# Optimization experiments

Measured on AMD Instinct MI355X. Metric: run time of the kernel, lower is better.

Reference implementation:

```python
import jax, jax.numpy as jnp
import numpy as np

B, N, D_IN, D_OUT, R = 8, 1024, 256, 256, 4


def setup_inputs() -> dict:
    key = jax.random.key(0)
    ks = jax.random.split(key, 8)
    scale_in = 1.0 / np.sqrt(D_IN)
    scale_out = 1.0 / np.sqrt(2 * D_OUT)
    scale_g = 1.0 / np.sqrt(D_OUT)
    return {
        "node_features": jax.random.normal(ks[0], (B, N, D_IN), dtype=jnp.float32),
        "adj_matrix": jax.random.randint(ks[1], (B, R, N, N), 0, 2, dtype=jnp.int32),
        "rel_w": jax.random.uniform(ks[2], (R, D_OUT, D_IN), jnp.float32, -scale_in, scale_in),
        "rel_b": jax.random.uniform(ks[3], (R, D_OUT), jnp.float32, -scale_in, scale_in),
        "attn_w": jax.random.uniform(ks[4], (2 * D_OUT,), jnp.float32, -scale_out, scale_out),
        "attn_b": jax.random.uniform(ks[5], (), jnp.float32, -scale_out, scale_out),
        "gate_w": jax.random.uniform(ks[6], (D_OUT,), jnp.float32, -scale_g, scale_g),
        "gate_b": jax.random.uniform(ks[7], (), jnp.float32, -scale_g, scale_g),
    }


def reference(node_features, adj_matrix, rel_w, rel_b, attn_w, attn_b, gate_w, gate_b):
    # Per-relation projections: [B, R, N, D]
    feats = jnp.einsum('bni,rdi->brnd', node_features, rel_w) + rel_b[None, :, None, :]
    # attn_proj(cat([h_i, h_j])) == h_i @ w_i + h_j @ w_j + b  (linear over concat)
    d = feats.shape[-1]
    si = jnp.einsum('brnd,d->brn', feats, attn_w[:d])   # contribution of row node i
    sj = jnp.einsum('brnd,d->brn', feats, attn_w[d:])   # contribution of col node j
    score = si[:, :, :, None] + sj[:, :, None, :] + attn_b  # [B, R, N, N]
    score = jnp.where(adj_matrix == 0, jnp.float32(-1e9), score)
    attn = jax.nn.softmax(score, axis=-1)
    # Aggregate over relations: sum_r attn_r @ feats_r -> [B, N, D]
    agg = jnp.einsum('brnm,brmd->bnd', attn, feats)
    gate = jax.nn.sigmoid(jnp.einsum('bnd,d->bn', agg, gate_w) + gate_b)
    return gate[:, :, None] * agg
```

## Files before the change

### kernel.cpp

```cpp
#include <hip/hip_runtime.h>
#include <hip/hip_bf16.h>

#define B_ 8
#define N_ 1024
#define DIN 256
#define DOUT 256
#define R_ 4

typedef __attribute__((ext_vector_type(8))) short bf16x8;
typedef __attribute__((ext_vector_type(4))) float f32x4;
typedef __attribute__((ext_vector_type(4))) int i32x4;

__device__ __forceinline__ unsigned short f2bf(float f) {
    union { float f; unsigned int u; } v; v.f = f;
    unsigned int u = v.u;
    u += 0x7fffu + ((u >> 16) & 1u);
    return (unsigned short)(u >> 16);
}
__device__ __forceinline__ float bf2f(unsigned short h) {
    union { float f; unsigned int u; } v; v.u = ((unsigned int)h) << 16;
    return v.f;
}

__device__ __forceinline__ void gl_lds16(const void* g, void* l) {
    __builtin_amdgcn_global_load_lds(
        (const __attribute__((address_space(1))) unsigned int*)g,
        (__attribute__((address_space(3))) unsigned int*)l, 16, 0, 0);
}

__global__ __launch_bounds__(256) void k0_swz(const float* __restrict__ rw,
                                              unsigned short* __restrict__ swzW) {
    int t = blockIdx.x * 256 + threadIdx.x;
    int lane = t & 63, nb = (t >> 6) & 15, ks = (t >> 10) & 7, r = t >> 13;
    int m = lane & 15, q = lane >> 4;
    const float* src = rw + ((r * DOUT + nb * 16 + m) * DIN) + ks * 32 + q * 8;
    float4 v0 = *(const float4*)src;
    float4 v1 = *(const float4*)(src + 4);
    bf16x8 o;
    o[0] = (short)f2bf(v0.x); o[1] = (short)f2bf(v0.y);
    o[2] = (short)f2bf(v0.z); o[3] = (short)f2bf(v0.w);
    o[4] = (short)f2bf(v1.x); o[5] = (short)f2bf(v1.y);
    o[6] = (short)f2bf(v1.z); o[7] = (short)f2bf(v1.w);
    *(bf16x8*)(swzW + (long)t * 8) = o;
}

__global__ __launch_bounds__(256) void k1_proj(const float* __restrict__ node,
        const unsigned short* __restrict__ swzW, const float* __restrict__ rel_b,
        const float* __restrict__ attn_w,
        unsigned short* __restrict__ fswz, unsigned short* __restrict__ ebf) {
    __shared__ unsigned short Wbuf[2][8192];
    int bid = blockIdx.x;
    int nt = bid & 15, r = (bid >> 4) & 3, b = bid >> 6;
    int w = threadIdx.x >> 6, lane = threadIdx.x & 63;
    int m = lane & 15, q = lane >> 4;
    int n0 = nt * 64 + w * 16;

    const float* Abase = node + ((b * N_ + n0 + m) * DIN) + q * 8;
    const unsigned short* Wsrc = swzW + r * 65536;

#pragma unroll
    for (int i = 0; i < 4; i++)
        gl_lds16(Wsrc + (w * 4 + i) * 512 + lane * 8, &Wbuf[0][(w * 4 + i) * 512]);

    f32x4 acc[16];
#pragma unroll
    for (int i = 0; i < 16; i++) acc[i] = (f32x4)0.0f;

    float4 a0 = *(const float4*)(Abase);
    float4 a1 = *(const float4*)(Abase + 4);

    for (int ks = 0; ks < 8; ks++) {
        int cur = ks & 1;
        __syncthreads();
        if (ks < 7) {
#pragma unroll
            for (int i = 0; i < 4; i++)
                gl_lds16(Wsrc + ((ks + 1) * 16 + w * 4 + i) * 512 + lane * 8,
                         &Wbuf[cur ^ 1][(w * 4 + i) * 512]);
        }
        bf16x8 af;
        af[0] = (short)f2bf(a0.x); af[1] = (short)f2bf(a0.y);
        af[2] = (short)f2bf(a0.z); af[3] = (short)f2bf(a0.w);
        af[4] = (short)f2bf(a1.x); af[5] = (short)f2bf(a1.y);
        af[6] = (short)f2bf(a1.z); af[7] = (short)f2bf(a1.w);
        if (ks < 7) {
            a0 = *(const float4*)(Abase + (ks + 1) * 32);
            a1 = *(const float4*)(Abase + (ks + 1) * 32 + 4);
        }
#pragma unroll
        for (int nb = 0; nb < 16; nb++) {
            bf16x8 wf = *(const bf16x8*)(&Wbuf[cur][nb * 512 + lane * 8]);
            acc[nb] = __builtin_amdgcn_mfma_f32_16x16x32_bf16(af, wf, acc[nb], 0, 0, 0);
        }
    }

    float sj0 = 0.f, sj1 = 0.f, sj2 = 0.f, sj3 = 0.f;
    float bias[16], aw[16];
#pragma unroll
    for (int nb = 0; nb < 16; nb++) {
        int d = nb * 16 + m;
        bias[nb] = rel_b[r * DOUT + d];
        aw[nb] = attn_w[DOUT + d];
        sj0 += (acc[nb][0] + bias[nb]) * aw[nb];
        sj1 += (acc[nb][1] + bias[nb]) * aw[nb];
        sj2 += (acc[nb][2] + bias[nb]) * aw[nb];
        sj3 += (acc[nb][3] + bias[nb]) * aw[nb];
    }
#pragma unroll
    for (int mk = 1; mk <= 8; mk <<= 1) {
        sj0 += __shfl_xor(sj0, mk, 64);
        sj1 += __shfl_xor(sj1, mk, 64);
        sj2 += __shfl_xor(sj2, mk, 64);
        sj3 += __shfl_xor(sj3, mk, 64);
    }
    float e0 = __expf(sj0), e1 = __expf(sj1), e2 = __expf(sj2), e3 = __expf(sj3);

    int slice = b * R_ + r;
    int js = n0 >> 5;
    int jhi = (n0 >> 4) & 1;
    int qp = jhi * 2 + (q >> 1);
    int jj0 = (q & 1) * 4;
    unsigned short* fb = fswz + ((long)(slice * 32 + js) * 16) * 512
                       + qp * 128 + m * 8 + jj0;
#pragma unroll
    for (int nb = 0; nb < 16; nb++) {
        ushort4 o;
        o.x = f2bf((acc[nb][0] + bias[nb]) * e0);
        o.y = f2bf((acc[nb][1] + bias[nb]) * e1);
        o.z = f2bf((acc[nb][2] + bias[nb]) * e2);
        o.w = f2bf((acc[nb][3] + bias[nb]) * e3);
        *(ushort4*)(fb + nb * 512) = o;
    }
    if (m == 0) {
        ushort4 o;
        o.x = f2bf(e0); o.y = f2bf(e1); o.z = f2bf(e2); o.w = f2bf(e3);
        *(ushort4*)(ebf + slice * N_ + n0 + q * 4) = o;
    }
}

__global__ __launch_bounds__(256, 4) void k3_attn(const int* __restrict__ adj,
        const unsigned short* __restrict__ fswz, const unsigned short* __restrict__ ebf,
        unsigned short* __restrict__ aggN) {
    __shared__ unsigned short Gbuf[2][8192];
    __shared__ unsigned short Ebuf[1024];
    __shared__ float Lx[2][64];

    int bid = blockIdx.x;
    int slice = (bid & 7) * 4 + ((bid >> 3) & 3);
    int it = bid >> 5;
    int t = threadIdx.x, lane = t & 63, w = t >> 6;
    int m = lane & 15, q = lane >> 4;
    int g = w & 1;
    int ph = w >> 1;
    int i0 = it * 32 + g * 16;

    const unsigned short* fsl = fswz + (size_t)slice * (32 * 8192);
    const int* adjbase = adj + (size_t)slice * (N_ * N_)
                       + (size_t)(i0 + m) * N_ + q * 8;
    const unsigned short* esl = ebf + slice * N_;

#pragma unroll
    for (int i = 0; i < 4; i++)
        gl_lds16(fsl + (w * 4 + i) * 512 + lane * 8, &Gbuf[0][(w * 4 + i) * 512]);
    if (w < 2)
        gl_lds16(esl + w * 512 + lane * 8, &Ebuf[w * 512]);

    i32x4 A0c = *(const i32x4*)(adjbase + ph * 32);
    i32x4 A1c = *(const i32x4*)(adjbase + ph * 32 + 4);

    f32x4 acc[16];
#pragma unroll
    for (int i = 0; i < 16; i++) acc[i] = (f32x4)0.0f;
    float l = 0.f;

    for (int s = 0; s < 32; s++) {
        int cur = s & 1;
        __syncthreads();
        if (s < 31) {
#pragma unroll
            for (int i = 0; i < 4; i++)
                gl_lds16(fsl + (size_t)(s + 1) * 8192 + (w * 4 + i) * 512 + lane * 8,
                         &Gbuf[cur ^ 1][(w * 4 + i) * 512]);
        }
        if ((s & 1) == ph) {
            i32x4 A0n, A1n;
            if (s < 30) {
                A0n = *(const i32x4*)(adjbase + (s + 2) * 32);
                A1n = *(const i32x4*)(adjbase + (s + 2) * 32 + 4);
            }
            bf16x8 ev = *(const bf16x8*)(&Ebuf[s * 32 + q * 8]);
            int av[8] = {A0c.x, A0c.y, A0c.z, A0c.w, A1c.x, A1c.y, A1c.z, A1c.w};
            const int* ei = (const int*)&ev;
            bf16x8 af;
            int* afi = (int*)&af;
#pragma unroll
            for (int p = 0; p < 4; p++) {
                unsigned int msk = (av[2 * p] ? 0xffffu : 0u)
                                 | (av[2 * p + 1] ? 0xffff0000u : 0u);
                afi[p] = (int)(msk & 0x3F803F80u);
                int me = ei[p] & (int)msk;
                union { int i; float f; } lo, hi;
                lo.i = me << 16;
                hi.i = me & (int)0xffff0000u;
                l += lo.f + hi.f;
            }
            const unsigned short* Gb = &Gbuf[cur][lane * 8];
#pragma unroll
            for (int nb = 0; nb < 16; nb++) {
                bf16x8 bfq = *(const bf16x8*)(Gb + nb * 512);
                acc[nb] = __builtin_amdgcn_mfma_f32_16x16x32_bf16(af, bfq, acc[nb], 0, 0, 0);
            }
            if (s < 30) { A0c = A0n; A1c = A1n; }
        }
    }

    __syncthreads();
    if (w >= 2) {
        float* GF = (float*)&Gbuf[0][0];
#pragma unroll
        for (int nb = 0; nb < 16; nb++)
            *(f32x4*)(&GF[g * 4096 + nb * 256 + lane * 4]) = acc[nb];
        Lx[g][lane] = l;
    }
    __syncthreads();
    if (w < 2) {
        const float* GF = (const float*)&Gbuf[0][0];
#pragma unroll
        for (int nb = 0; nb < 16; nb++)
            acc[nb] += *(const f32x4*)(&GF[g * 4096 + nb * 256 + lane * 4]);
        l += Lx[g][lane];
        l += __shfl_xor(l, 16, 64);
        l += __shfl_xor(l, 32, 64);
        float linv[4];
#pragma unroll
        for (int reg = 0; reg < 4; reg++) {
            float lr = __shfl(l, q * 4 + reg, 64);
            linv[reg] = (lr > 0.f) ? 1.0f / lr : 0.f;
        }
        unsigned short* ob = aggN + ((size_t)(slice * N_ + i0 + q * 4)) * DOUT + m;
#pragma unroll
        for (int nb = 0; nb < 16; nb++) {
#pragma unroll
            for (int reg = 0; reg < 4; reg++)
                ob[(size_t)reg * DOUT + nb * 16] = f2bf(acc[nb][reg] * linv[reg]);
        }
    }
}

__global__ __launch_bounds__(256) void k4_out(const unsigned short* __restrict__ aggN,
        const float* __restrict__ gate_w, const float* __restrict__ gate_b,
        float* __restrict__ out) {
    __shared__ float red[4];
    int bid = blockIdx.x;
    int n = bid & 1023, b = bid >> 10;
    int d = threadIdx.x;
    float s = 0.f;
#pragma unroll
    for (int r = 0; r < R_; r++)
        s += bf2f(aggN[((size_t)((b * R_ + r) * N_ + n)) * DOUT + d]);
    float v = s * gate_w[d];
#pragma unroll
    for (int off = 32; off; off >>= 1) v += __shfl_down(v, off, 64);
    int lane = d & 63, wave = d >> 6;
    if (lane == 0) red[wave] = v;
    __syncthreads();
    float tot = red[0] + red[1] + red[2] + red[3];
    float g = 1.f / (1.f + __expf(-(tot + gate_b[0])));
    out[((size_t)(b * N_ + n)) * DOUT + d] = g * s;
}

extern "C" void kernel_launch(void* const* d_in, const int* in_sizes, int n_in,
                              void* d_out, int out_size, void* d_ws, size_t ws_size,
                              hipStream_t stream) {
    const float* node   = (const float*)d_in[0];
    const int*   adj    = (const int*)d_in[1];
    const float* rel_w  = (const float*)d_in[2];
    const float* rel_b  = (const float*)d_in[3];
    const float* attn_w = (const float*)d_in[4];
    const float* gate_w = (const float*)d_in[6];
    const float* gate_b = (const float*)d_in[7];
    float* out = (float*)d_out;

    char* ws = (char*)d_ws;
    unsigned short* swzW = (unsigned short*)ws;
    unsigned short* fswz = (unsigned short*)(ws + 524288);
    unsigned short* ebf  = (unsigned short*)(ws + 17301504);
    unsigned short* aggN = (unsigned short*)(ws + 17367040);

    k0_swz<<<128, 256, 0, stream>>>(rel_w, swzW);
    k1_proj<<<512, 256, 0, stream>>>(node, swzW, rel_b, attn_w, fswz, ebf);
    k3_attn<<<1024, 256, 0, stream>>>(adj, fswz, ebf, aggN);
    k4_out<<<8192, 256, 0, stream>>>(aggN, gate_w, gate_b, out);
}
```

Baseline: 257.1 us.

## Restructure attention kernel: 64 rows per block, 4-slot pipeline with vmcnt waits

The attention kernel now gives each of its four waves a distinct 16-row tile, so a block covers 64 rows and the grid is halved. This replaces the old scheme where pairs of waves split the column steps and then merged partial sums through shared memory. Feature tiles and adjacency loads move into a 4-slot LDS/register ring, prefetched two steps ahead. Manual s_waitcnt vmcnt plus raw barriers replace __syncthreads so loads in flight can stay pending. Each fswz tile is now reused across more rows, at the cost of more LDS per block (occupancy bound lowered to 2) and fragile hand-counted waitcnt logic.

```diff
diff --git a/kernel.cpp b/kernel.cpp
--- a/kernel.cpp
+++ b/kernel.cpp
@@ -26,6 +26,12 @@
     __builtin_amdgcn_global_load_lds(
         (const __attribute__((address_space(1))) unsigned int*)g,
         (__attribute__((address_space(3))) unsigned int*)l, 16, 0, 0);
+}
+
+__device__ __forceinline__ i32x4 gload4(const void* p) {
+    i32x4 r;
+    asm volatile("global_load_dwordx4 %0, %1, off" : "=v"(r) : "v"(p) : "memory");
+    return r;
 }
 
 __global__ __launch_bounds__(256) void k0_swz(const float* __restrict__ rw,
@@ -138,112 +144,105 @@
     }
 }
 
-__global__ __launch_bounds__(256, 4) void k3_attn(const int* __restrict__ adj,
+#define K3_STEP(T_, SLOT_, PFSLOT_, DO_PF_, WAITN_)                            \
+  {                                                                            \
+    asm volatile("s_waitcnt vmcnt(" #WAITN_ ")" ::: "memory");                 \
+    __builtin_amdgcn_s_barrier();                                              \
+    __builtin_amdgcn_sched_barrier(0);                                         \
+    if (DO_PF_) {                                                              \
+      _Pragma("unroll")                                                        \
+      for (int i = 0; i < 4; i++)                                              \
+        gl_lds16(fsl + (size_t)((T_) + 2) * 8192 + (w * 4 + i) * 512 + lane * 8, \
+                 &Gbuf[PFSLOT_][(w * 4 + i) * 512]);                           \
+      adjA[PFSLOT_] = gload4(adjbase + ((T_) + 2) * 32);                       \
+      adjB[PFSLOT_] = gload4(adjbase + ((T_) + 2) * 32 + 4);                   \
+    }                                                                          \
+    bf16x8 ev = *(const bf16x8*)(&Ebuf[(T_) * 32 + q * 8]);                    \
+    i32x4 A0c = adjA[SLOT_], A1c = adjB[SLOT_];                                \
+    int av[8] = {A0c.x, A0c.y, A0c.z, A0c.w, A1c.x, A1c.y, A1c.z, A1c.w};      \
+    const int* ei = (const int*)&ev;                                           \
+    bf16x8 af; int* afi = (int*)&af;                                           \
+    _Pragma("unroll")                                                          \
+    for (int p = 0; p < 4; p++) {                                              \
+      unsigned int msk = (av[2 * p] ? 0xffffu : 0u)                            \
+                       | (av[2 * p + 1] ? 0xffff0000u : 0u);                   \
+      afi[p] = (int)(msk & 0x3F803F80u);                                       \
+      int me = ei[p] & (int)msk;                                               \
+      union { int i; float f; } lo, hi;                                        \
+      lo.i = me << 16; hi.i = me & (int)0xffff0000u;                           \
+      l += lo.f + hi.f;                                                        \
+    }                                                                          \
+    const unsigned short* Gb = &Gbuf[SLOT_][lane * 8];                         \
+    _Pragma("unroll")                                                          \
+    for (int nb = 0; nb < 16; nb++) {                                          \
+      bf16x8 bfq = *(const bf16x8*)(Gb + nb * 512);                            \
+      acc[nb] = __builtin_amdgcn_mfma_f32_16x16x32_bf16(af, bfq, acc[nb], 0, 0, 0); \
+    }                                                                          \
+  }
+
+__global__ __launch_bounds__(256, 2) void k3_attn(const int* __restrict__ adj,
         const unsigned short* __restrict__ fswz, const unsigned short* __restrict__ ebf,
         unsigned short* __restrict__ aggN) {
-    __shared__ unsigned short Gbuf[2][8192];
+    __shared__ unsigned short Gbuf[4][8192];
     __shared__ unsigned short Ebuf[1024];
-    __shared__ float Lx[2][64];
 
     int bid = blockIdx.x;
     int slice = (bid & 7) * 4 + ((bid >> 3) & 3);
     int it = bid >> 5;
     int t = threadIdx.x, lane = t & 63, w = t >> 6;
     int m = lane & 15, q = lane >> 4;
-    int g = w & 1;
-    int ph = w >> 1;
-    int i0 = it * 32 + g * 16;
+    int i0 = it * 64 + w * 16;
 
     const unsigned short* fsl = fswz + (size_t)slice * (32 * 8192);
     const int* adjbase = adj + (size_t)slice * (N_ * N_)
                        + (size_t)(i0 + m) * N_ + q * 8;
     const unsigned short* esl = ebf + slice * N_;
 
+    i32x4 adjA[4], adjB[4];
+
 #pragma unroll
     for (int i = 0; i < 4; i++)
         gl_lds16(fsl + (w * 4 + i) * 512 + lane * 8, &Gbuf[0][(w * 4 + i) * 512]);
     if (w < 2)
         gl_lds16(esl + w * 512 + lane * 8, &Ebuf[w * 512]);
-
-    i32x4 A0c = *(const i32x4*)(adjbase + ph * 32);
-    i32x4 A1c = *(const i32x4*)(adjbase + ph * 32 + 4);
+    adjA[0] = gload4(adjbase);
+    adjB[0] = gload4(adjbase + 4);
+#pragma unroll
+    for (int i = 0; i < 4; i++)
+        gl_lds16(fsl + 8192 + (w * 4 + i) * 512 + lane * 8, &Gbuf[1][(w * 4 + i) * 512]);
+    adjA[1] = gload4(adjbase + 32);
+    adjB[1] = gload4(adjbase + 36);
 
     f32x4 acc[16];
 #pragma unroll
     for (int i = 0; i < 16; i++) acc[i] = (f32x4)0.0f;
     float l = 0.f;
 
-    for (int s = 0; s < 32; s++) {
-        int cur = s & 1;
-        __syncthreads();
-        if (s < 31) {
-#pragma unroll
-            for (int i = 0; i < 4; i++)
-                gl_lds16(fsl + (size_t)(s + 1) * 8192 + (w * 4 + i) * 512 + lane * 8,
-                         &Gbuf[cur ^ 1][(w * 4 + i) * 512]);
-        }
-        if ((s & 1) == ph) {
-            i32x4 A0n, A1n;
-            if (s < 30) {
-                A0n = *(const i32x4*)(adjbase + (s + 2) * 32);
-                A1n = *(const i32x4*)(adjbase + (s + 2) * 32 + 4);
-            }
-            bf16x8 ev = *(const bf16x8*)(&Ebuf[s * 32 + q * 8]);
-            int av[8] = {A0c.x, A0c.y, A0c.z, A0c.w, A1c.x, A1c.y, A1c.z, A1c.w};
-            const int* ei = (const int*)&ev;
-            bf16x8 af;
-            int* afi = (int*)&af;
-#pragma unroll
-            for (int p = 0; p < 4; p++) {
-                unsigned int msk = (av[2 * p] ? 0xffffu : 0u)
-                                 | (av[2 * p + 1] ? 0xffff0000u : 0u);
-                afi[p] = (int)(msk & 0x3F803F80u);
-                int me = ei[p] & (int)msk;
-                union { int i; float f; } lo, hi;
-                lo.i = me << 16;
-                hi.i = me & (int)0xffff0000u;
-                l += lo.f + hi.f;
-            }
-            const unsigned short* Gb = &Gbuf[cur][lane * 8];
-#pragma unroll
-            for (int nb = 0; nb < 16; nb++) {
-                bf16x8 bfq = *(const bf16x8*)(Gb + nb * 512);
-                acc[nb] = __builtin_amdgcn_mfma_f32_16x16x32_bf16(af, bfq, acc[nb], 0, 0, 0);
-            }
-            if (s < 30) { A0c = A0n; A1c = A1n; }
-        }
-    }
-
-    __syncthreads();
-    if (w >= 2) {
-        float* GF = (float*)&Gbuf[0][0];
-#pragma unroll
-        for (int nb = 0; nb < 16; nb++)
-            *(f32x4*)(&GF[g * 4096 + nb * 256 + lane * 4]) = acc[nb];
-        Lx[g][lane] = l;
-    }
-    __syncthreads();
-    if (w < 2) {
-        const float* GF = (const float*)&Gbuf[0][0];
-#pragma unroll
-        for (int nb = 0; nb < 16; nb++)
-            acc[nb] += *(const f32x4*)(&GF[g * 4096 + nb * 256 + lane * 4]);
-        l += Lx[g][lane];
-        l += __shfl_xor(l, 16, 64);
-        l += __shfl_xor(l, 32, 64);
-        float linv[4];
-#pragma unroll
-        for (int reg = 0; reg < 4; reg++) {
-            float lr = __shfl(l, q * 4 + reg, 64);
-            linv[reg] = (lr > 0.f) ? 1.0f / lr : 0.f;
-        }
-        unsigned short* ob = aggN + ((size_t)(slice * N_ + i0 + q * 4)) * DOUT + m;
-#pragma unroll
-        for (int nb = 0; nb < 16; nb++) {
-#pragma unroll
-            for (int reg = 0; reg < 4; reg++)
-                ob[(size_t)reg * DOUT + nb * 16] = f2bf(acc[nb][reg] * linv[reg]);
-        }
+    for (int tt = 0; tt < 28; tt += 4) {
+        K3_STEP(tt + 0, 0, 2, 1, 6)
+        K3_STEP(tt + 1, 1, 3, 1, 6)
+        K3_STEP(tt + 2, 2, 0, 1, 6)
+        K3_STEP(tt + 3, 3, 1, 1, 6)
+    }
+    K3_STEP(28, 0, 2, 1, 6)
+    K3_STEP(29, 1, 3, 1, 6)
+    K3_STEP(30, 2, 0, 0, 6)
+    K3_STEP(31, 3, 1, 0, 0)
+
+    l += __shfl_xor(l, 16, 64);
+    l += __shfl_xor(l, 32, 64);
+    float linv[4];
+#pragma unroll
+    for (int reg = 0; reg < 4; reg++) {
+        float lr = __shfl(l, q * 4 + reg, 64);
+        linv[reg] = (lr > 0.f) ? 1.0f / lr : 0.f;
+    }
+    unsigned short* ob = aggN + ((size_t)(slice * N_ + i0 + q * 4)) * DOUT + m;
+#pragma unroll
+    for (int nb = 0; nb < 16; nb++) {
+#pragma unroll
+        for (int reg = 0; reg < 4; reg++)
+            ob[(size_t)reg * DOUT + nb * 16] = f2bf(acc[nb][reg] * linv[reg]);
     }
 }
 
@@ -289,6 +288,6 @@
 
     k0_swz<<<128, 256, 0, stream>>>(rel_w, swzW);
     k1_proj<<<512, 256, 0, stream>>>(node, swzW, rel_b, attn_w, fswz, ebf);
-    k3_attn<<<1024, 256, 0, stream>>>(adj, fswz, ebf, aggN);
+    k3_attn<<<512, 256, 0, stream>>>(adj, fswz, ebf, aggN);
     k4_out<<<8192, 256, 0, stream>>>(aggN, gate_w, gate_b, out);
 }
```

New measurement: 251.6 us. -2.2%, faster.

## Restructure attention kernel: each wave owns 16 rows, read features directly from global

Applied to the files above, without the earlier changes.

The attention aggregation kernel is reorganised so that each of the four waves handles its own 16 query rows across all 32 key tiles. This removes the split-K phase scheme, the cross-wave LDS reduction and the per-step barriers. Feature tiles are now read straight from global memory (relying on L2/cache) instead of being double-buffered through LDS. The grid is halved to 512 blocks and the occupancy hint drops to 2. This trades LDS traffic and synchronisation for more redundant global/L2 reads of the features per block and less latency hiding.

```diff
diff --git a/kernel.cpp b/kernel.cpp
--- a/kernel.cpp
+++ b/kernel.cpp
@@ -138,112 +138,78 @@
     }
 }
 
-__global__ __launch_bounds__(256, 4) void k3_attn(const int* __restrict__ adj,
+__global__ __launch_bounds__(256, 2) void k3_attn(const int* __restrict__ adj,
         const unsigned short* __restrict__ fswz, const unsigned short* __restrict__ ebf,
         unsigned short* __restrict__ aggN) {
-    __shared__ unsigned short Gbuf[2][8192];
     __shared__ unsigned short Ebuf[1024];
-    __shared__ float Lx[2][64];
 
     int bid = blockIdx.x;
     int slice = (bid & 7) * 4 + ((bid >> 3) & 3);
     int it = bid >> 5;
     int t = threadIdx.x, lane = t & 63, w = t >> 6;
     int m = lane & 15, q = lane >> 4;
-    int g = w & 1;
-    int ph = w >> 1;
-    int i0 = it * 32 + g * 16;
+    int i0 = it * 64 + w * 16;
 
     const unsigned short* fsl = fswz + (size_t)slice * (32 * 8192);
     const int* adjbase = adj + (size_t)slice * (N_ * N_)
                        + (size_t)(i0 + m) * N_ + q * 8;
-    const unsigned short* esl = ebf + slice * N_;
-
-#pragma unroll
-    for (int i = 0; i < 4; i++)
-        gl_lds16(fsl + (w * 4 + i) * 512 + lane * 8, &Gbuf[0][(w * 4 + i) * 512]);
-    if (w < 2)
-        gl_lds16(esl + w * 512 + lane * 8, &Ebuf[w * 512]);
-
-    i32x4 A0c = *(const i32x4*)(adjbase + ph * 32);
-    i32x4 A1c = *(const i32x4*)(adjbase + ph * 32 + 4);
+
+    ((ushort4*)Ebuf)[t] = ((const ushort4*)(ebf + slice * N_))[t];
+    __syncthreads();
 
     f32x4 acc[16];
 #pragma unroll
     for (int i = 0; i < 16; i++) acc[i] = (f32x4)0.0f;
     float l = 0.f;
 
+    i32x4 A0c = *(const i32x4*)(adjbase);
+    i32x4 A1c = *(const i32x4*)(adjbase + 4);
+
     for (int s = 0; s < 32; s++) {
-        int cur = s & 1;
-        __syncthreads();
+        i32x4 A0n, A1n;
         if (s < 31) {
-#pragma unroll
-            for (int i = 0; i < 4; i++)
-                gl_lds16(fsl + (size_t)(s + 1) * 8192 + (w * 4 + i) * 512 + lane * 8,
-                         &Gbuf[cur ^ 1][(w * 4 + i) * 512]);
-        }
-        if ((s & 1) == ph) {
-            i32x4 A0n, A1n;
-            if (s < 30) {
-                A0n = *(const i32x4*)(adjbase + (s + 2) * 32);
-                A1n = *(const i32x4*)(adjbase + (s + 2) * 32 + 4);
-            }
-            bf16x8 ev = *(const bf16x8*)(&Ebuf[s * 32 + q * 8]);
-            int av[8] = {A0c.x, A0c.y, A0c.z, A0c.w, A1c.x, A1c.y, A1c.z, A1c.w};
-            const int* ei = (const int*)&ev;
-            bf16x8 af;
-            int* afi = (int*)&af;
-#pragma unroll
-            for (int p = 0; p < 4; p++) {
-                unsigned int msk = (av[2 * p] ? 0xffffu : 0u)
-                                 | (av[2 * p + 1] ? 0xffff0000u : 0u);
-                afi[p] = (int)(msk & 0x3F803F80u);
-                int me = ei[p] & (int)msk;
-                union { int i; float f; } lo, hi;
-                lo.i = me << 16;
-                hi.i = me & (int)0xffff0000u;
-                l += lo.f + hi.f;
-            }
-            const unsigned short* Gb = &Gbuf[cur][lane * 8];
-#pragma unroll
-            for (int nb = 0; nb < 16; nb++) {
-                bf16x8 bfq = *(const bf16x8*)(Gb + nb * 512);
-                acc[nb] = __builtin_amdgcn_mfma_f32_16x16x32_bf16(af, bfq, acc[nb], 0, 0, 0);
-            }
-            if (s < 30) { A0c = A0n; A1c = A1n; }
-        }
-    }
-
-    __syncthreads();
-    if (w >= 2) {
-        float* GF = (float*)&Gbuf[0][0];
-#pragma unroll
-        for (int nb = 0; nb < 16; nb++)
-            *(f32x4*)(&GF[g * 4096 + nb * 256 + lane * 4]) = acc[nb];
-        Lx[g][lane] = l;
-    }
-    __syncthreads();
-    if (w < 2) {
-        const float* GF = (const float*)&Gbuf[0][0];
-#pragma unroll
-        for (int nb = 0; nb < 16; nb++)
-            acc[nb] += *(const f32x4*)(&GF[g * 4096 + nb * 256 + lane * 4]);
-        l += Lx[g][lane];
-        l += __shfl_xor(l, 16, 64);
-        l += __shfl_xor(l, 32, 64);
-        float linv[4];
-#pragma unroll
-        for (int reg = 0; reg < 4; reg++) {
-            float lr = __shfl(l, q * 4 + reg, 64);
-            linv[reg] = (lr > 0.f) ? 1.0f / lr : 0.f;
-        }
-        unsigned short* ob = aggN + ((size_t)(slice * N_ + i0 + q * 4)) * DOUT + m;
+            A0n = *(const i32x4*)(adjbase + (s + 1) * 32);
+            A1n = *(const i32x4*)(adjbase + (s + 1) * 32 + 4);
+        }
+        bf16x8 ev = *(const bf16x8*)(&Ebuf[s * 32 + q * 8]);
+        int av[8] = {A0c.x, A0c.y, A0c.z, A0c.w, A1c.x, A1c.y, A1c.z, A1c.w};
+        const int* ei = (const int*)&ev;
+        bf16x8 af;
+        int* afi = (int*)&af;
+#pragma unroll
+        for (int p = 0; p < 4; p++) {
+            unsigned int msk = (av[2 * p] ? 0xffffu : 0u)
+                             | (av[2 * p + 1] ? 0xffff0000u : 0u);
+            afi[p] = (int)(msk & 0x3F803F80u);
+            int me = ei[p] & (int)msk;
+            union { int i; float f; } lo, hi;
+            lo.i = me << 16;
+            hi.i = me & (int)0xffff0000u;
+            l += lo.f + hi.f;
+        }
+        const bf16x8* Gp = (const bf16x8*)(fsl + (size_t)s * 8192) + lane;
 #pragma unroll
         for (int nb = 0; nb < 16; nb++) {
-#pragma unroll
-            for (int reg = 0; reg < 4; reg++)
-                ob[(size_t)reg * DOUT + nb * 16] = f2bf(acc[nb][reg] * linv[reg]);
-        }
+            bf16x8 bfq = Gp[nb * 64];
+            acc[nb] = __builtin_amdgcn_mfma_f32_16x16x32_bf16(af, bfq, acc[nb], 0, 0, 0);
+        }
+        A0c = A0n; A1c = A1n;
+    }
+
+    l += __shfl_xor(l, 16, 64);
+    l += __shfl_xor(l, 32, 64);
+    float linv[4];
+#pragma unroll
+    for (int reg = 0; reg < 4; reg++) {
+        float lr = __shfl(l, q * 4 + reg, 64);
+        linv[reg] = (lr > 0.f) ? 1.0f / lr : 0.f;
+    }
+    unsigned short* ob = aggN + ((size_t)(slice * N_ + i0 + q * 4)) * DOUT + m;
+#pragma unroll
+    for (int nb = 0; nb < 16; nb++) {
+#pragma unroll
+        for (int reg = 0; reg < 4; reg++)
+            ob[(size_t)reg * DOUT + nb * 16] = f2bf(acc[nb][reg] * linv[reg]);
     }
 }
 
@@ -289,6 +255,6 @@
 
     k0_swz<<<128, 256, 0, stream>>>(rel_w, swzW);
     k1_proj<<<512, 256, 0, stream>>>(node, swzW, rel_b, attn_w, fswz, ebf);
-    k3_attn<<<1024, 256, 0, stream>>>(adj, fswz, ebf, aggN);
+    k3_attn<<<512, 256, 0, stream>>>(adj, fswz, ebf, aggN);
     k4_out<<<8192, 256, 0, stream>>>(aggN, gate_w, gate_b, out);
 }
```

Result: no change. 262.0 us (+1.9%).
